# Kernel optimization log

Measured on AMD Instinct MI355X. Metric: run time of the kernel, lower is better.

Reference implementation:

```python
import jax, jax.numpy as jnp
import numpy as np

N, E, D, H = 50000, 500000, 128, 4
HD = D // H
LN_EPS = 1e-5


def _layernorm(z, g, b):
    mu = jnp.mean(z, axis=-1, keepdims=True)
    var = jnp.mean(jnp.square(z - mu), axis=-1, keepdims=True)
    return (z - mu) * jax.lax.rsqrt(var + LN_EPS) * g + b


def setup_inputs() -> dict:
    key = jax.random.key(0)
    ks = jax.random.split(key, 10)
    s = 1.0 / np.sqrt(D)
    return {
        "x": jax.random.normal(ks[0], (N, D), jnp.float32),
        "edge_index": jax.random.randint(ks[1], (2, E), 0, N, jnp.int32),
        "edge_attr": jax.random.normal(ks[2], (E, D), jnp.float32),
        "W_l": jax.random.normal(ks[3], (D, D), jnp.float32) * s,
        "b_l": jnp.zeros((D,), jnp.float32),
        "W_r": jax.random.normal(ks[4], (D, D), jnp.float32) * s,
        "b_r": jnp.zeros((D,), jnp.float32),
        "W_e": jax.random.normal(ks[5], (D, D), jnp.float32) * s,
        "b_e": jnp.zeros((D,), jnp.float32),
        "att": jax.random.normal(ks[6], (H, HD), jnp.float32) * s,
        "bias": jnp.zeros((D,), jnp.float32),
        "ln_g": jnp.ones((2 * D,), jnp.float32),
        "ln_b": jnp.zeros((2 * D,), jnp.float32),
        "W_mlp": jax.random.normal(ks[7], (2 * D, D), jnp.float32) * (1.0 / np.sqrt(2 * D)),
        "b_mlp": jnp.zeros((D,), jnp.float32),
    }


def reference(x, edge_index, edge_attr, W_l, b_l, W_r, b_r, W_e, b_e, att,
              bias, ln_g, ln_b, W_mlp, b_mlp):
    n = x.shape[0]
    src, dst = edge_index[0], edge_index[1]
    # GATv2Conv (heads=H, concat=True, edge_dim=D)
    xl = (x @ W_l + b_l).reshape(n, H, HD)          # lin_l(x)
    xr = (x @ W_r + b_r).reshape(n, H, HD)          # lin_r(x)
    ee = (edge_attr @ W_e + b_e).reshape(-1, H, HD)  # lin_edge(edge_attr)
    m = xl[src] + xr[dst] + ee                       # [E,H,HD]
    e = jnp.sum(jax.nn.leaky_relu(m, 0.2) * att, axis=-1)  # [E,H]
    emax = jax.ops.segment_max(e, dst, num_segments=n)
    emax = jax.lax.stop_gradient(jnp.where(jnp.isfinite(emax), emax, 0.0))
    ex = jnp.exp(e - emax[dst])
    denom = jax.ops.segment_sum(ex, dst, num_segments=n)
    alpha = ex / (denom[dst] + 1e-16)                # segment softmax over incoming edges
    agg = jax.ops.segment_sum(alpha[..., None] * xl[src], dst, num_segments=n)
    x_new = agg.reshape(n, H * HD) + bias            # [N,D]
    # edgeMLP: gather -> concat -> LayerNorm -> ReLU -> Linear -> residual add
    cat = jnp.concatenate([x_new[src], x_new[dst]], axis=-1)  # [E,2D]
    h = jax.nn.relu(_layernorm(cat, ln_g, ln_b))
    edge_attr_new = edge_attr + h @ W_mlp + b_mlp
    return x_new, edge_attr_new
```

## Files before the change

### kernel.cpp

```cpp
#include <hip/hip_runtime.h>
#include <math.h>

typedef float  f32x4  __attribute__((ext_vector_type(4)));
typedef __bf16 bf16x8 __attribute__((ext_vector_type(8)));

union FragU { uint4 q; bf16x8 b; };

__device__ inline float fc(const float4& v, int k){
  return k==0 ? v.x : k==1 ? v.y : k==2 ? v.z : v.w;
}

__global__ void k_pack(const float* __restrict__ Wl, const float* __restrict__ Wr,
                       const float* __restrict__ We, const float* __restrict__ Wm,
                       const float* __restrict__ lng, const float* __restrict__ lnb,
                       unsigned short* plr, unsigned short* pe, unsigned short* pm,
                       unsigned short* plnb){
  int t = blockIdx.x * 256 + threadIdx.x;
  if (t < 32768){
    int j = t & 7, lane = (t >> 3) & 63, ks = (t >> 9) & 3, ct = t >> 11;
    int k = ks*32 + (lane >> 4)*8 + j, c = ct*16 + (lane & 15);
    float v = (c < 128) ? Wl[k*128 + c] : Wr[k*128 + (c - 128)];
    __bf16 b = (__bf16)v; plr[t] = *(unsigned short*)&b;
  }
  if (t < 16384){
    int j = t & 7, lane = (t >> 3) & 63, ks = (t >> 9) & 3, ct = t >> 11;
    int k = ks*32 + (lane >> 4)*8 + j, c = ct*16 + (lane & 15);
    __bf16 b = (__bf16)We[k*128 + c]; pe[t] = *(unsigned short*)&b;
  }
  if (t < 32768){
    int j = t & 7, lane = (t >> 3) & 63, ks = (t >> 9) & 7, ct = t >> 12;
    int k = ks*32 + (lane >> 4)*8 + j, c = ct*16 + (lane & 15);
    __bf16 b = (__bf16)Wm[k*128 + c]; pm[t] = *(unsigned short*)&b;
  }
  if (t < 512){
    float v = (t < 256) ? lng[t] : lnb[t-256];
    __bf16 b = (__bf16)v; plnb[t] = *(unsigned short*)&b;
  }
}

__global__ void k_scan1(const int* __restrict__ cnt, int* __restrict__ pre,
                        int* __restrict__ bsum, int n){
  __shared__ int wsum[4];
  int t = threadIdx.x, lane = t & 63, w = t >> 6;
  int base = blockIdx.x*1024 + t*4;
  int v[4]; int loc = 0;
  #pragma unroll
  for (int j = 0; j < 4; ++j){ v[j] = (base+j < n) ? cnt[base+j] : 0; loc += v[j]; }
  int incl = loc;
  #pragma unroll
  for (int o = 1; o < 64; o <<= 1){
    int u = __shfl_up(incl, o);
    if (lane >= o) incl += u;
  }
  if (lane == 63) wsum[w] = incl;
  __syncthreads();
  int wbase = 0;
  #pragma unroll
  for (int ww = 0; ww < 4; ++ww) if (ww < w) wbase += wsum[ww];
  int run = wbase + incl - loc;
  #pragma unroll
  for (int j = 0; j < 4; ++j){ if (base+j < n) pre[base+j] = run; run += v[j]; }
  if (t == 255) bsum[blockIdx.x] = wbase + incl;
}

__global__ void k_scan2(const int* __restrict__ bsum, int* __restrict__ boff, int nb){
  int t = threadIdx.x;
  int v = (t < nb) ? bsum[t] : 0;
  int incl = v;
  #pragma unroll
  for (int o = 1; o < 64; o <<= 1){
    int u = __shfl_up(incl, o);
    if (t >= o) incl += u;
  }
  if (t < nb) boff[t] = incl - v;
  if (t == nb-1) boff[nb] = incl;
}

__global__ void k_scan3(const int* __restrict__ pre, const int* __restrict__ boff,
                        int* __restrict__ rowptr, int* __restrict__ cursor, int n, int nb){
  int i = blockIdx.x*256 + threadIdx.x;
  if (i < n){
    int r = pre[i] + boff[blockIdx.x >> 2];
    rowptr[i] = r; cursor[i] = r;
  }
  if (i == 0) rowptr[n] = boff[nb];
}

__global__ void k_scatter(const int* __restrict__ dst, int* __restrict__ cursor,
                          int* __restrict__ eids, int E){
  int e = blockIdx.x*256 + threadIdx.x;
  if (e < E){ int p = atomicAdd(&cursor[dst[e]], 1); eids[p] = e; }
}

__launch_bounds__(512)
__global__ void k_node_linear(const float* __restrict__ x, const float* __restrict__ bl,
                              const float* __restrict__ br, const unsigned short* __restrict__ plr,
                              __bf16* __restrict__ xlxr, int n){
  __shared__ uint4 sW[4096];
  int t = threadIdx.x, lane = t & 63, w = t >> 6, lo = lane & 15, hi = lane >> 4;
  for (int i = t; i < 4096; i += 512) sW[i] = ((const uint4*)plr)[i];
  int row = blockIdx.x*128 + w*16 + lo;
  int rc  = min(row, n-1);
  bf16x8 A[4];
  #pragma unroll
  for (int ks = 0; ks < 4; ++ks){
    const float* p = &x[(size_t)rc*128 + ks*32 + hi*8];
    float4 v0 = *(const float4*)p, v1 = *(const float4*)(p+4);
    FragU u;
    u.b[0]=(__bf16)v0.x; u.b[1]=(__bf16)v0.y; u.b[2]=(__bf16)v0.z; u.b[3]=(__bf16)v0.w;
    u.b[4]=(__bf16)v1.x; u.b[5]=(__bf16)v1.y; u.b[6]=(__bf16)v1.z; u.b[7]=(__bf16)v1.w;
    A[ks] = u.b;
  }
  __syncthreads();
  f32x4 acc[16];
  #pragma unroll
  for (int ct = 0; ct < 16; ++ct) acc[ct] = (f32x4)(0.f);
  #pragma unroll
  for (int ks = 0; ks < 4; ++ks){
    #pragma unroll
    for (int ct = 0; ct < 16; ++ct){
      FragU bu; bu.q = sW[(ct*4 + ks)*64 + lane];
      acc[ct] = __builtin_amdgcn_mfma_f32_16x16x32_bf16(A[ks], bu.b, acc[ct], 0, 0, 0);
    }
  }
  float biasL[16];
  #pragma unroll
  for (int ct = 0; ct < 16; ++ct){
    int c = ct*16 + lo;
    biasL[ct] = (c < 128) ? bl[c] : br[c - 128];
  }
  #pragma unroll
  for (int j = 0; j < 4; ++j){
    int nd = blockIdx.x*128 + w*16 + hi*4 + j;
    if (nd < n){
      #pragma unroll
      for (int ct = 0; ct < 16; ++ct)
        xlxr[(size_t)nd*256 + ct*16 + lo] = (__bf16)(acc[ct][j] + biasL[ct]);
    }
  }
}

__launch_bounds__(512)
__global__ void k_edge_logits(const float* __restrict__ eattr, const int* __restrict__ src,
                              const int* __restrict__ dst, const unsigned short* __restrict__ pe,
                              const float* __restrict__ be, const float* __restrict__ att,
                              const __bf16* __restrict__ xlxr, float* __restrict__ elog,
                              int* __restrict__ cnt, int E){
  __shared__ uint4 sW[2048];
  int t = threadIdx.x, lane = t & 63, w = t >> 6, lo = lane & 15, hi = lane >> 4;
  for (int i = t; i < 2048; i += 512) sW[i] = ((const uint4*)pe)[i];
  int eb = blockIdx.x*128 + w*16;
  int er = min(eb + lo, E-1);
  bf16x8 A[4];
  #pragma unroll
  for (int ks = 0; ks < 4; ++ks){
    const float* p = &eattr[(size_t)er*128 + ks*32 + hi*8];
    f32x4 v0 = __builtin_nontemporal_load((const f32x4*)p);
    f32x4 v1 = __builtin_nontemporal_load((const f32x4*)(p+4));
    FragU u;
    u.b[0]=(__bf16)v0[0]; u.b[1]=(__bf16)v0[1]; u.b[2]=(__bf16)v0[2]; u.b[3]=(__bf16)v0[3];
    u.b[4]=(__bf16)v1[0]; u.b[5]=(__bf16)v1[1]; u.b[6]=(__bf16)v1[2]; u.b[7]=(__bf16)v1[3];
    A[ks] = u.b;
  }
  __syncthreads();
  f32x4 acc[8];
  #pragma unroll
  for (int ct = 0; ct < 8; ++ct) acc[ct] = (f32x4)(0.f);
  #pragma unroll
  for (int ks = 0; ks < 4; ++ks){
    #pragma unroll
    for (int ct = 0; ct < 8; ++ct){
      FragU bu; bu.q = sW[(ct*4 + ks)*64 + lane];
      acc[ct] = __builtin_amdgcn_mfma_f32_16x16x32_bf16(A[ks], bu.b, acc[ct], 0, 0, 0);
    }
  }
  float beL[8], atL[8];
  #pragma unroll
  for (int ct = 0; ct < 8; ++ct){ beL[ct] = be[ct*16 + lo]; atL[ct] = att[ct*16 + lo]; }
  #pragma unroll
  for (int j = 0; j < 4; ++j){
    int e = eb + hi*4 + j;
    int ec = min(e, E-1);
    int s_ = src[ec], d_ = dst[ec];
    const __bf16* xlp = &xlxr[(size_t)s_*256];
    const __bf16* xrp = &xlxr[(size_t)d_*256 + 128];
    float qh[4];
    #pragma unroll
    for (int h = 0; h < 4; ++h){
      float p = 0.f;
      #pragma unroll
      for (int u = 0; u < 2; ++u){
        int ct = 2*h + u, c = ct*16 + lo;
        float m = acc[ct][j] + beL[ct] + (float)xlp[c] + (float)xrp[c];
        m = (m > 0.f) ? m : 0.2f*m;
        p = fmaf(m, atL[ct], p);
      }
      p += __shfl_xor(p, 1); p += __shfl_xor(p, 2);
      p += __shfl_xor(p, 4); p += __shfl_xor(p, 8);
      qh[h] = p;
    }
    if (lo == 0 && e < E){
      *(float4*)&elog[(size_t)e*4] = make_float4(qh[0], qh[1], qh[2], qh[3]);
      atomicAdd(&cnt[d_], 1);
    }
  }
}

__launch_bounds__(256)
__global__ void k_gat_agg(const float* __restrict__ elog, const int* __restrict__ rowptr,
                          const int* __restrict__ eids, const int* __restrict__ src,
                          const __bf16* __restrict__ xlxr, const float* __restrict__ bias,
                          float* __restrict__ xnew, __bf16* __restrict__ xnb,
                          float2* __restrict__ nstat, int n){
  int nd = (blockIdx.x*256 + threadIdx.x) >> 6;
  int lane = threadIdx.x & 63;
  if (nd >= n) return;
  int beg = rowptr[nd], end = rowptr[nd+1];
  bool hsel = (lane & 32) != 0;
  float m0 = -INFINITY, m1 = -INFINITY, d0 = 0.f, d1 = 0.f;
  for (int i = beg; i < end; ++i){
    float4 lv = *(const float4*)&elog[(size_t)eids[i]*4];
    float l0 = hsel ? lv.y : lv.x, l1 = hsel ? lv.w : lv.z;
    float nm0 = fmaxf(m0, l0), nm1 = fmaxf(m1, l1);
    d0 = d0*__expf(m0 - nm0) + __expf(l0 - nm0);
    d1 = d1*__expf(m1 - nm1) + __expf(l1 - nm1);
    m0 = nm0; m1 = nm1;
  }
  float r0 = 1.f/(d0 + 1e-16f), r1 = 1.f/(d1 + 1e-16f);
  float a0 = 0.f, a1 = 0.f;
  int c0 = lane, c1 = lane + 64;
  for (int i = beg; i < end; ++i){
    int e = eids[i];
    float4 lv = *(const float4*)&elog[(size_t)e*4];
    float l0 = hsel ? lv.y : lv.x, l1 = hsel ? lv.w : lv.z;
    float al0 = __expf(l0 - m0)*r0, al1 = __expf(l1 - m1)*r1;
    const __bf16* xp = &xlxr[(size_t)src[e]*256];
    a0 = fmaf(al0, (float)xp[c0], a0);
    a1 = fmaf(al1, (float)xp[c1], a1);
  }
  float v0 = a0 + bias[c0], v1 = a1 + bias[c1];
  xnew[(size_t)nd*128 + c0] = v0;
  xnew[(size_t)nd*128 + c1] = v1;
  xnb[(size_t)nd*128 + c0] = (__bf16)v0;
  xnb[(size_t)nd*128 + c1] = (__bf16)v1;
  float s  = v0 + v1;
  float ss = fmaf(v0, v0, v1*v1);
  #pragma unroll
  for (int o = 1; o < 64; o <<= 1){ s += __shfl_xor(s, o); ss += __shfl_xor(ss, o); }
  if (lane == 0) nstat[nd] = make_float2(s, ss);
}

__launch_bounds__(512, 4)
__global__ void k_edge_mlp(const __bf16* __restrict__ xnb, const int* __restrict__ src,
                           const int* __restrict__ dst, const float* __restrict__ eattr,
                           const unsigned short* __restrict__ pm, const float* __restrict__ bmlp,
                           const unsigned short* __restrict__ plnb,
                           const float2* __restrict__ nstat, float* __restrict__ out, int E){
  __shared__ uint4 sW[4096];
  __shared__ __align__(16) unsigned short sLN[512];
  const uint4* pm_q = (const uint4*)pm;
  int t = threadIdx.x, lane = t & 63, w = t >> 6, lo = lane & 15, hi = lane >> 4;
  int base = blockIdx.x*128;
  float ev[4][8];
  #pragma unroll
  for (int j = 0; j < 4; ++j){
    int e2 = min(base + w*16 + hi*4 + j, E-1);
    const float* ep = &eattr[(size_t)e2*128 + lo];
    #pragma unroll
    for (int ct = 0; ct < 8; ++ct)
      ev[j][ct] = __builtin_nontemporal_load(ep + ct*16);
  }
  for (int i = t; i < 4096; i += 512) sW[i] = pm_q[i];
  if (t < 512) sLN[t] = plnb[t];
  int e  = base + w*16 + lo;
  int ec = min(e, E-1);
  int s_ = src[ec], d_ = dst[ec];
  float2 stS = nstat[s_], stD = nstat[d_];
  float mean = (stS.x + stD.x) * (1.f/256.f);
  float var  = (stS.y + stD.y) * (1.f/256.f) - mean*mean;
  float rstd = rsqrtf(var + 1e-5f);
  const __bf16* srow = &xnb[(size_t)s_*128 + hi*8];
  const __bf16* drow = &xnb[(size_t)d_*128 + hi*8];
  uint4 g[8];
  #pragma unroll
  for (int ks = 0; ks < 4; ++ks){
    g[ks]   = *(const uint4*)&srow[ks*32];
    g[4+ks] = *(const uint4*)&drow[ks*32];
  }
  __syncthreads();
  bf16x8 af[8];
  #pragma unroll
  for (int ks = 0; ks < 8; ++ks){
    int cb = ks*32 + hi*8;
    FragU u, a, lg, lb;
    u.q  = g[ks];
    lg.q = *(const uint4*)&sLN[cb];
    lb.q = *(const uint4*)&sLN[256 + cb];
    #pragma unroll
    for (int j = 0; j < 8; ++j){
      float v = fmaxf(fmaf(((float)u.b[j] - mean)*rstd, (float)lg.b[j], (float)lb.b[j]), 0.f);
      a.b[j] = (__bf16)v;
    }
    af[ks] = a.b;
  }
  f32x4 acc[8];
  #pragma unroll
  for (int ct = 0; ct < 8; ++ct) acc[ct] = (f32x4)(0.f);
  #pragma unroll
  for (int ks = 0; ks < 8; ++ks){
    #pragma unroll
    for (int ct = 0; ct < 8; ++ct){
      FragU bu; bu.q = sW[(ct*8 + ks)*64 + lane];
      acc[ct] = __builtin_amdgcn_mfma_f32_16x16x32_bf16(af[ks], bu.b, acc[ct], 0, 0, 0);
    }
  }
  float bmL[8];
  #pragma unroll
  for (int ct = 0; ct < 8; ++ct) bmL[ct] = bmlp[ct*16 + lo];
  #pragma unroll
  for (int j = 0; j < 4; ++j){
    int e2 = base + w*16 + hi*4 + j;
    if (e2 < E){
      #pragma unroll
      for (int ct = 0; ct < 8; ++ct){
        int c = ct*16 + lo;
        __builtin_nontemporal_store(acc[ct][j] + bmL[ct] + ev[j][ct],
                                    &out[(size_t)e2*128 + c]);
      }
    }
  }
}

extern "C" void kernel_launch(void* const* d_in, const int* in_sizes, int n_in,
                              void* d_out, int out_size, void* d_ws, size_t ws_size,
                              hipStream_t stream){
  const float* x     = (const float*)d_in[0];
  const int*   eidx  = (const int*)  d_in[1];
  const float* eattr = (const float*)d_in[2];
  const float* Wl    = (const float*)d_in[3];
  const float* bl    = (const float*)d_in[4];
  const float* Wr    = (const float*)d_in[5];
  const float* br    = (const float*)d_in[6];
  const float* We    = (const float*)d_in[7];
  const float* be    = (const float*)d_in[8];
  const float* att   = (const float*)d_in[9];
  const float* bias  = (const float*)d_in[10];
  const float* lng   = (const float*)d_in[11];
  const float* lnb   = (const float*)d_in[12];
  const float* Wmlp  = (const float*)d_in[13];
  const float* bmlp  = (const float*)d_in[14];

  int n = in_sizes[0] / 128;
  int E = in_sizes[2] / 128;
  const int* src = eidx;
  const int* dst = eidx + E;
  int nb = (n + 1023) / 1024;

  char* ws = (char*)d_ws;
  size_t off = 0;
  int* cnt    = (int*)(ws + off); off += (size_t)n*4;
  size_t zbytes = off;
  int* pre    = (int*)(ws + off); off += (size_t)n*4;
  int* rowptr = (int*)(ws + off); off += (size_t)(n+1)*4;
  int* cursor = (int*)(ws + off); off += (size_t)(n+1)*4;
  int* bsum   = (int*)(ws + off); off += (size_t)nb*4;
  int* boff   = (int*)(ws + off); off += (size_t)(nb+1)*4;
  int* eids   = (int*)(ws + off); off += (size_t)E*4;
  __bf16* xlxr = (__bf16*)(ws + off); off += (size_t)n*256*2;
  float* elog = (float*)(ws + off); off += (size_t)E*4*4;
  float2* nstat = (float2*)(ws + off); off += (size_t)n*8;
  __bf16* xnb = (__bf16*)(ws + off); off += (size_t)n*128*2;
  unsigned short* plr = (unsigned short*)(ws + off); off += 32768*2;
  unsigned short* pe  = (unsigned short*)(ws + off); off += 16384*2;
  unsigned short* pm  = (unsigned short*)(ws + off); off += 32768*2;
  unsigned short* plnb= (unsigned short*)(ws + off); off += 512*2;

  float* xnew_out = (float*)d_out;
  float* eout     = (float*)d_out + (size_t)n*128;

  hipMemsetAsync(ws, 0, zbytes, stream);
  k_pack       <<<128, 256, 0, stream>>>(Wl, Wr, We, Wmlp, lng, lnb, plr, pe, pm, plnb);
  k_node_linear<<<(n + 127)/128, 512, 0, stream>>>(x, bl, br, plr, xlxr, n);
  k_edge_logits<<<(E + 127)/128, 512, 0, stream>>>(eattr, src, dst, pe, be, att, xlxr, elog, cnt, E);
  k_scan1      <<<nb, 256, 0, stream>>>(cnt, pre, bsum, n);
  k_scan2      <<<1, 64, 0, stream>>>(bsum, boff, nb);
  k_scan3      <<<nb*4, 256, 0, stream>>>(pre, boff, rowptr, cursor, n, nb);
  k_scatter    <<<(E + 255)/256, 256, 0, stream>>>(dst, cursor, eids, E);
  k_gat_agg    <<<(n + 3)/4, 256, 0, stream>>>(elog, rowptr, eids, src, xlxr, bias, xnew_out, xnb, nstat, n);
  k_edge_mlp   <<<(E + 127)/128, 512, 0, stream>>>(xnb, src, dst, eattr, pm, bmlp, plnb, nstat, eout, E);
}
```

Measured before the change: 445.0 us.

## Process two edge tiles per MLP block and vectorize GAT aggregation lanes

The edge MLP kernel now handles EPB=2 tiles of 128 edges per block. This spreads the 64KB shared-memory weight load over twice as many edges and halves the block count. The GAT aggregation kernel switches to one head per 16-lane group, with each lane owning two adjacent columns. That allows paired bf16 loads and packed float2/uint stores and drops the duplicated two-head softmax tracking. The risks are less parallelism and little overlap between the tile loads and the MFMA work inside a block.

After: 510.2 us. 14.7% more time.

```diff
diff --git a/kernel.cpp b/kernel.cpp
--- a/kernel.cpp
+++ b/kernel.cpp
@@ -5,6 +5,8 @@
 typedef __bf16 bf16x8 __attribute__((ext_vector_type(8)));
 
 union FragU { uint4 q; bf16x8 b; };
+
+#define EPB 2
 
 __device__ inline float fc(const float4& v, int k){
   return k==0 ? v.x : k==1 ? v.y : k==2 ? v.z : v.w;
@@ -216,33 +218,32 @@
   int lane = threadIdx.x & 63;
   if (nd >= n) return;
   int beg = rowptr[nd], end = rowptr[nd+1];
-  bool hsel = (lane & 32) != 0;
-  float m0 = -INFINITY, m1 = -INFINITY, d0 = 0.f, d1 = 0.f;
+  int c0 = 2*lane;
+  int h  = lane >> 4;
+  float m = -INFINITY, d = 0.f;
   for (int i = beg; i < end; ++i){
     float4 lv = *(const float4*)&elog[(size_t)eids[i]*4];
-    float l0 = hsel ? lv.y : lv.x, l1 = hsel ? lv.w : lv.z;
-    float nm0 = fmaxf(m0, l0), nm1 = fmaxf(m1, l1);
-    d0 = d0*__expf(m0 - nm0) + __expf(l0 - nm0);
-    d1 = d1*__expf(m1 - nm1) + __expf(l1 - nm1);
-    m0 = nm0; m1 = nm1;
-  }
-  float r0 = 1.f/(d0 + 1e-16f), r1 = 1.f/(d1 + 1e-16f);
+    float l = (h & 2) ? ((h & 1) ? lv.w : lv.z) : ((h & 1) ? lv.y : lv.x);
+    float nm = fmaxf(m, l);
+    d = d*__expf(m - nm) + __expf(l - nm);
+    m = nm;
+  }
+  float r = 1.f/(d + 1e-16f);
   float a0 = 0.f, a1 = 0.f;
-  int c0 = lane, c1 = lane + 64;
   for (int i = beg; i < end; ++i){
     int e = eids[i];
     float4 lv = *(const float4*)&elog[(size_t)e*4];
-    float l0 = hsel ? lv.y : lv.x, l1 = hsel ? lv.w : lv.z;
-    float al0 = __expf(l0 - m0)*r0, al1 = __expf(l1 - m1)*r1;
-    const __bf16* xp = &xlxr[(size_t)src[e]*256];
-    a0 = fmaf(al0, (float)xp[c0], a0);
-    a1 = fmaf(al1, (float)xp[c1], a1);
-  }
-  float v0 = a0 + bias[c0], v1 = a1 + bias[c1];
-  xnew[(size_t)nd*128 + c0] = v0;
-  xnew[(size_t)nd*128 + c1] = v1;
-  xnb[(size_t)nd*128 + c0] = (__bf16)v0;
-  xnb[(size_t)nd*128 + c1] = (__bf16)v1;
+    float l = (h & 2) ? ((h & 1) ? lv.w : lv.z) : ((h & 1) ? lv.y : lv.x);
+    float al = __expf(l - m)*r;
+    unsigned u = *(const unsigned*)&xlxr[(size_t)src[e]*256 + c0];
+    a0 = fmaf(al, __uint_as_float(u << 16),        a0);
+    a1 = fmaf(al, __uint_as_float(u & 0xffff0000u), a1);
+  }
+  float v0 = a0 + bias[c0], v1 = a1 + bias[c0+1];
+  *(float2*)&xnew[(size_t)nd*128 + c0] = make_float2(v0, v1);
+  __bf16 b0 = (__bf16)v0, b1 = (__bf16)v1;
+  unsigned up = (unsigned)(*(unsigned short*)&b0) | ((unsigned)(*(unsigned short*)&b1) << 16);
+  *(unsigned*)&xnb[(size_t)nd*128 + c0] = up;
   float s  = v0 + v1;
   float ss = fmaf(v0, v0, v1*v1);
   #pragma unroll
@@ -260,11 +261,15 @@
   __shared__ __align__(16) unsigned short sLN[512];
   const uint4* pm_q = (const uint4*)pm;
   int t = threadIdx.x, lane = t & 63, w = t >> 6, lo = lane & 15, hi = lane >> 4;
-  int base = blockIdx.x*128;
+  int base0 = blockIdx.x * 128 * EPB;
+
   float ev[4][8];
+  uint4 g[8];
+  float2 stS, stD;
+
   #pragma unroll
   for (int j = 0; j < 4; ++j){
-    int e2 = min(base + w*16 + hi*4 + j, E-1);
+    int e2 = min(base0 + w*16 + hi*4 + j, E-1);
     const float* ep = &eattr[(size_t)e2*128 + lo];
     #pragma unroll
     for (int ct = 0; ct < 8; ++ct)
@@ -272,60 +277,86 @@
   }
   for (int i = t; i < 4096; i += 512) sW[i] = pm_q[i];
   if (t < 512) sLN[t] = plnb[t];
-  int e  = base + w*16 + lo;
-  int ec = min(e, E-1);
-  int s_ = src[ec], d_ = dst[ec];
-  float2 stS = nstat[s_], stD = nstat[d_];
-  float mean = (stS.x + stD.x) * (1.f/256.f);
-  float var  = (stS.y + stD.y) * (1.f/256.f) - mean*mean;
-  float rstd = rsqrtf(var + 1e-5f);
-  const __bf16* srow = &xnb[(size_t)s_*128 + hi*8];
-  const __bf16* drow = &xnb[(size_t)d_*128 + hi*8];
-  uint4 g[8];
-  #pragma unroll
-  for (int ks = 0; ks < 4; ++ks){
-    g[ks]   = *(const uint4*)&srow[ks*32];
-    g[4+ks] = *(const uint4*)&drow[ks*32];
+  {
+    int ec = min(base0 + w*16 + lo, E-1);
+    int s_ = src[ec], d_ = dst[ec];
+    stS = nstat[s_]; stD = nstat[d_];
+    const __bf16* srow = &xnb[(size_t)s_*128 + hi*8];
+    const __bf16* drow = &xnb[(size_t)d_*128 + hi*8];
+    #pragma unroll
+    for (int ks = 0; ks < 4; ++ks){
+      g[ks]   = *(const uint4*)&srow[ks*32];
+      g[4+ks] = *(const uint4*)&drow[ks*32];
+    }
   }
   __syncthreads();
-  bf16x8 af[8];
-  #pragma unroll
-  for (int ks = 0; ks < 8; ++ks){
-    int cb = ks*32 + hi*8;
-    FragU u, a, lg, lb;
-    u.q  = g[ks];
-    lg.q = *(const uint4*)&sLN[cb];
-    lb.q = *(const uint4*)&sLN[256 + cb];
-    #pragma unroll
-    for (int j = 0; j < 8; ++j){
-      float v = fmaxf(fmaf(((float)u.b[j] - mean)*rstd, (float)lg.b[j], (float)lb.b[j]), 0.f);
-      a.b[j] = (__bf16)v;
-    }
-    af[ks] = a.b;
-  }
-  f32x4 acc[8];
-  #pragma unroll
-  for (int ct = 0; ct < 8; ++ct) acc[ct] = (f32x4)(0.f);
-  #pragma unroll
-  for (int ks = 0; ks < 8; ++ks){
-    #pragma unroll
-    for (int ct = 0; ct < 8; ++ct){
-      FragU bu; bu.q = sW[(ct*8 + ks)*64 + lane];
-      acc[ct] = __builtin_amdgcn_mfma_f32_16x16x32_bf16(af[ks], bu.b, acc[ct], 0, 0, 0);
-    }
-  }
+
   float bmL[8];
   #pragma unroll
   for (int ct = 0; ct < 8; ++ct) bmL[ct] = bmlp[ct*16 + lo];
-  #pragma unroll
-  for (int j = 0; j < 4; ++j){
-    int e2 = base + w*16 + hi*4 + j;
-    if (e2 < E){
+
+  #pragma unroll
+  for (int tt = 0; tt < EPB; ++tt){
+    int base = base0 + tt*128;
+    if (tt > 0){
+      #pragma unroll
+      for (int j = 0; j < 4; ++j){
+        int e2 = min(base + w*16 + hi*4 + j, E-1);
+        const float* ep = &eattr[(size_t)e2*128 + lo];
+        #pragma unroll
+        for (int ct = 0; ct < 8; ++ct)
+          ev[j][ct] = __builtin_nontemporal_load(ep + ct*16);
+      }
+      int ec = min(base + w*16 + lo, E-1);
+      int s_ = src[ec], d_ = dst[ec];
+      stS = nstat[s_]; stD = nstat[d_];
+      const __bf16* srow = &xnb[(size_t)s_*128 + hi*8];
+      const __bf16* drow = &xnb[(size_t)d_*128 + hi*8];
+      #pragma unroll
+      for (int ks = 0; ks < 4; ++ks){
+        g[ks]   = *(const uint4*)&srow[ks*32];
+        g[4+ks] = *(const uint4*)&drow[ks*32];
+      }
+    }
+    float mean = (stS.x + stD.x) * (1.f/256.f);
+    float var  = (stS.y + stD.y) * (1.f/256.f) - mean*mean;
+    float rstd = rsqrtf(var + 1e-5f);
+    bf16x8 af[8];
+    #pragma unroll
+    for (int ks = 0; ks < 8; ++ks){
+      int cb = ks*32 + hi*8;
+      FragU u, a, lg, lb;
+      u.q  = g[ks];
+      lg.q = *(const uint4*)&sLN[cb];
+      lb.q = *(const uint4*)&sLN[256 + cb];
+      #pragma unroll
+      for (int j = 0; j < 8; ++j){
+        float v = fmaxf(fmaf(((float)u.b[j] - mean)*rstd, (float)lg.b[j], (float)lb.b[j]), 0.f);
+        a.b[j] = (__bf16)v;
+      }
+      af[ks] = a.b;
+    }
+    f32x4 acc[8];
+    #pragma unroll
+    for (int ct = 0; ct < 8; ++ct) acc[ct] = (f32x4)(0.f);
+    #pragma unroll
+    for (int ks = 0; ks < 8; ++ks){
       #pragma unroll
       for (int ct = 0; ct < 8; ++ct){
-        int c = ct*16 + lo;
-        __builtin_nontemporal_store(acc[ct][j] + bmL[ct] + ev[j][ct],
-                                    &out[(size_t)e2*128 + c]);
+        FragU bu; bu.q = sW[(ct*8 + ks)*64 + lane];
+        acc[ct] = __builtin_amdgcn_mfma_f32_16x16x32_bf16(af[ks], bu.b, acc[ct], 0, 0, 0);
+      }
+    }
+    #pragma unroll
+    for (int j = 0; j < 4; ++j){
+      int e2 = base + w*16 + hi*4 + j;
+      if (e2 < E){
+        #pragma unroll
+        for (int ct = 0; ct < 8; ++ct){
+          int c = ct*16 + lo;
+          __builtin_nontemporal_store(acc[ct][j] + bmL[ct] + ev[j][ct],
+                                      &out[(size_t)e2*128 + c]);
+        }
       }
     }
   }
@@ -387,5 +418,6 @@
   k_scan3      <<<nb*4, 256, 0, stream>>>(pre, boff, rowptr, cursor, n, nb);
   k_scatter    <<<(E + 255)/256, 256, 0, stream>>>(dst, cursor, eids, E);
   k_gat_agg    <<<(n + 3)/4, 256, 0, stream>>>(elog, rowptr, eids, src, xlxr, bias, xnew_out, xnb, nstat, n);
-  k_edge_mlp   <<<(E + 127)/128, 512, 0, stream>>>(xnb, src, dst, eattr, pm, bmlp, plnb, nstat, eout, E);
-}
+  int mlpb = (E + 128*EPB - 1) / (128*EPB);
+  k_edge_mlp   <<<mlpb, 512, 0, stream>>>(xnb, src, dst, eattr, pm, bmlp, plnb, nstat, eout, E);
+}
```
